# Optimization experiments

Hardware: AMD Instinct MI355X
Metric: run time of the kernel (lower is better)

Reference implementation:

```python
import jax, jax.numpy as jnp
import numpy as np

N_NODES = 100000
N_EDGES = 3200000
N_GRAPHS = 128
F_IN, HID, N_CLS = 3, 64, 6


def setup_inputs() -> dict:
    key = jax.random.key(0)
    ks = jax.random.split(key, 9)
    x = jax.random.normal(ks[0], (N_NODES, F_IN), dtype=jnp.float32)
    edge_index = jax.random.randint(ks[1], (2, N_EDGES), 0, N_NODES, dtype=jnp.int32)
    batch = jnp.sort(jax.random.randint(ks[2], (N_NODES,), 0, N_GRAPHS, dtype=jnp.int32))
    # GCNConv weights (glorot-ish) and biases
    W1 = jax.random.normal(ks[3], (F_IN, HID), dtype=jnp.float32) / np.float32(np.sqrt(F_IN))
    b1 = jnp.zeros((HID,), dtype=jnp.float32)
    W2 = jax.random.normal(ks[4], (HID, HID), dtype=jnp.float32) / np.float32(np.sqrt(HID))
    b2 = jnp.zeros((HID,), dtype=jnp.float32)
    Wl = jax.random.normal(ks[5], (HID, N_CLS), dtype=jnp.float32) / np.float32(np.sqrt(HID))
    bl = jnp.zeros((N_CLS,), dtype=jnp.float32)
    return {"x": x, "edge_index": edge_index, "batch": batch,
            "W1": W1, "b1": b1, "W2": W2, "b2": b2, "Wl": Wl, "bl": bl}


def _gcn_forward(x, edge_index, batch, W1, b1, W2, b2, Wl, bl):
    n = x.shape[0]
    # add self-loops (PyG GCNConv default)
    loop = jnp.arange(n, dtype=edge_index.dtype)
    src = jnp.concatenate([edge_index[0], loop])
    dst = jnp.concatenate([edge_index[1], loop])
    # symmetric normalization D^{-1/2} (A+I) D^{-1/2}
    deg = jax.ops.segment_sum(jnp.ones_like(dst, dtype=x.dtype), dst, num_segments=n)
    dis = jax.lax.rsqrt(jnp.maximum(deg, 1.0))
    norm = dis[src] * dis[dst]  # [E+N]

    def conv(h, W, b):
        h = h @ W                                   # [N, out]
        msg = h[src] * norm[:, None]                # gather + scale
        agg = jax.ops.segment_sum(msg, dst, num_segments=n)  # scatter-add
        return agg + b

    h = jax.nn.relu(conv(x, W1, b1))
    h = jax.nn.relu(conv(h, W2, b2))
    # global mean pool over graphs
    ones = jnp.ones((n,), dtype=h.dtype)
    cnt = jax.ops.segment_sum(ones, batch, num_segments=N_GRAPHS)
    pooled = jax.ops.segment_sum(h, batch, num_segments=N_GRAPHS) / jnp.maximum(cnt, 1.0)[:, None]
    logits = pooled @ Wl + bl
    return jax.nn.log_softmax(logits, axis=1)


def reference(x, edge_index, batch, W1, b1, W2, b2, Wl, bl):
    return _gcn_forward(x, edge_index, batch, W1, b1, W2, b2, Wl, bl)
```

## Files before the change

### kernel.cpp

```cpp
#include <hip/hip_runtime.h>
#include <math.h>

#define NGRAPH 128
#define NPB 128
#define CAPB 6144
#define PSL 8
#define MMN 16
#define TILEA 16384
#define EPTA 16


__device__ inline unsigned char f2fp8(float f) {
    float a = fabsf(f);
    unsigned s = (__float_as_uint(f) >> 31) << 7;
    if (!(a > 0.f)) return (unsigned char)s;
    if (a >= 448.f) return (unsigned char)(s | 0x7e);
    int e = (int)(__float_as_uint(a) >> 23) - 127;
    if (e < -6) e = -6;
    float sc = __uint_as_float((unsigned)(130 - e) << 23);
    int q = (int)rintf(a * sc);
    if (q >= 16) { e += 1; q = 8; }
    if (q <= 0) return (unsigned char)s;
    unsigned expb, man;
    if (q < 8) { expb = 0; man = (unsigned)q; }
    else { expb = (unsigned)(e + 7); man = (unsigned)(q - 8); }
    return (unsigned char)(s | (expb << 3) | man);
}

typedef float v2f __attribute__((ext_vector_type(2)));

__device__ inline void fp8x4_dec(unsigned u, float* o) {
#pragma unroll
    for (int k = 0; k < 4; ++k) {
        unsigned b = (u >> (8 * k)) & 0xffu;
        unsigned bits = ((b & 0x80u) << 24) | ((b & 0x7fu) << 20);
        o[k] = __uint_as_float(bits) * 0x1p+120f;
    }
}

__device__ inline void acc16(uint4 u, float w, v2f* a) {
#if __has_builtin(__builtin_amdgcn_cvt_pk_f32_fp8)
    v2f ws; ws.x = w; ws.y = w;
    a[0] += __builtin_amdgcn_cvt_pk_f32_fp8(u.x, false) * ws;
    a[1] += __builtin_amdgcn_cvt_pk_f32_fp8(u.x, true)  * ws;
    a[2] += __builtin_amdgcn_cvt_pk_f32_fp8(u.y, false) * ws;
    a[3] += __builtin_amdgcn_cvt_pk_f32_fp8(u.y, true)  * ws;
    a[4] += __builtin_amdgcn_cvt_pk_f32_fp8(u.z, false) * ws;
    a[5] += __builtin_amdgcn_cvt_pk_f32_fp8(u.z, true)  * ws;
    a[6] += __builtin_amdgcn_cvt_pk_f32_fp8(u.w, false) * ws;
    a[7] += __builtin_amdgcn_cvt_pk_f32_fp8(u.w, true)  * ws;
#else
    float* af = (float*)a;
    unsigned uu[4] = {u.x, u.y, u.z, u.w};
#pragma unroll
    for (int q = 0; q < 4; ++q) {
        float d[4]; fp8x4_dec(uu[q], d);
#pragma unroll
        for (int k = 0; k < 4; ++k) af[q * 4 + k] += d[k] * w;
    }
#endif
}


__global__ void init_k(int* __restrict__ cursorF, float* __restrict__ pooled, int NBF) {
    int i = blockIdx.x * blockDim.x + threadIdx.x;
    if (i < NBF) cursorF[i] = i * CAPB;
    if (i < NGRAPH * 64) pooled[i] = 0.0f;
}


__global__ __launch_bounds__(1024) void binA_k(const int* __restrict__ src,
        const int* __restrict__ dst, int* cursorF, unsigned* __restrict__ binned,
        int E, int NBF) {
    __shared__ int lh[1024];
    __shared__ int startv[1024];
    __shared__ int gdelta[1024];
    __shared__ unsigned lout[TILEA];
    int tid = threadIdx.x;
    lh[tid] = 0;
    __syncthreads();
    int base = blockIdx.x * TILEA;
    int d[EPTA];
    int s[EPTA];
#pragma unroll
    for (int u = 0; u < EPTA; ++u) {
        int e = base + tid + u * 1024;
        d[u] = (e < E) ? dst[e] : -1;
        s[u] = (e < E) ? src[e] : 0;
    }
#pragma unroll
    for (int u = 0; u < EPTA; ++u)
        if (d[u] >= 0) atomicAdd(&lh[d[u] >> 7], 1);
    __syncthreads();
    if (tid <= NBF) startv[tid] = (tid == 0) ? 0 : lh[tid - 1];
    __syncthreads();
    for (int off = 1; off <= NBF; off <<= 1) {
        int v = 0;
        if (tid <= NBF && tid >= off) v = startv[tid - off];
        __syncthreads();
        if (tid <= NBF && tid >= off) startv[tid] += v;
        __syncthreads();
    }
    if (tid < NBF) {
        int cnt = lh[tid];
        int g = cnt ? atomicAdd(&cursorF[tid], cnt) : 0;
        gdelta[tid] = g - startv[tid];
        lh[tid] = startv[tid];
    }
    __syncthreads();
#pragma unroll
    for (int u = 0; u < EPTA; ++u) {
        if (d[u] >= 0) {
            int p = atomicAdd(&lh[d[u] >> 7], 1);
            lout[p] = (unsigned)s[u] | ((unsigned)(d[u] & (NPB - 1)) << 17);
        }
    }
    __syncthreads();
    int wv = tid >> 6, ln = tid & 63;
    for (int bkt = wv; bkt < NBF; bkt += 16) {
        int ls = startv[bkt], le = lh[bkt];
        int gd = gdelta[bkt];
        for (int i = ls + ln; i < le; i += 64)
            binned[gd + i] = lout[i];
    }
}


__global__ __launch_bounds__(256) void reorder_k(unsigned* __restrict__ binned,
        const int* __restrict__ cursorF, int* __restrict__ nodebeg,
        int* __restrict__ nodeend, float* __restrict__ dis,
        const float* __restrict__ x, float* __restrict__ xs, int n) {
    __shared__ int hist[NPB + 1];
    __shared__ int startv[NPB + 1];
    __shared__ unsigned lout[CAPB];
    int tid = threadIdx.x;
    int b = blockIdx.x;
    int beg = b * CAPB, end = cursorF[b];
    int total = end - beg;
    if (tid <= NPB) hist[tid] = 0;
    __syncthreads();
    for (int i = beg + tid; i < end; i += 256)
        atomicAdd(&hist[binned[i] >> 17], 1);
    __syncthreads();
    if (tid < NPB) startv[tid + 1] = hist[tid];
    if (tid == 0) startv[0] = 0;
    __syncthreads();
    for (int off = 1; off <= NPB; off <<= 1) {
        int v = 0;
        if (tid <= NPB && tid >= off) v = startv[tid - off];
        __syncthreads();
        if (tid <= NPB && tid >= off) startv[tid] += v;
        __syncthreads();
    }
    if (tid < NPB) hist[tid] = startv[tid];
    __syncthreads();
    for (int i = beg + tid; i < end; i += 256) {
        unsigned r = binned[i];
        int p = atomicAdd(&hist[r >> 17], 1);
        lout[p] = r & 0x1FFFFu;
    }
    __syncthreads();
    for (int jj = tid; jj < total; jj += 256)
        binned[beg + jj] = lout[jj];
    int node0 = b * NPB;
    if (tid < NPB) {
        int node = node0 + tid;
        if (node < n) {
            nodebeg[node] = beg + startv[tid];
            nodeend[node] = beg + startv[tid + 1];
            int deg = startv[tid + 1] - startv[tid];
            float d = rsqrtf((float)deg + 1.0f);
            dis[node] = d;
            xs[node * 3]     = x[node * 3] * d;
            xs[node * 3 + 1] = x[node * 3 + 1] * d;
            xs[node * 3 + 2] = x[node * 3 + 2] * d;
        }
    }
}


__global__ __launch_bounds__(256) void mm12_k(const float* __restrict__ xs,
        const int* __restrict__ nodebeg, const int* __restrict__ nodeend,
        const int* __restrict__ csr, const float* __restrict__ dis,
        const float* __restrict__ W1, const float* __restrict__ b1,
        const float* __restrict__ W2, unsigned char* __restrict__ tb, int n) {
    __shared__ __attribute__((aligned(16))) float hrow[4][64];
    __shared__ float4 ytile[MMN];
    int tid = threadIdx.x;
    int j = tid & 63;

    float w1r0 = W1[j], w1r1 = W1[64 + j], w1r2 = W1[128 + j], bbr = b1[j];
    float wreg[64];
#pragma unroll
    for (int k = 0; k < 64; ++k) wreg[k] = W2[k * 64 + j];

    int ns = tid >> 4;
    int el = tid & 15;
    int gnode = blockIdx.x * MMN + ns;
    float a0 = 0.f, a1 = 0.f, a2 = 0.f;
    float dn = 0.f;
    int b = 0, e = 0;
    if (gnode < n) {
        dn = dis[gnode];
        b = nodebeg[gnode];
        e = nodeend[gnode];
    }
    for (int i = b + el; i < e; i += 32) {
        int s0 = csr[i];
        int i1 = i + 16;
        bool v1 = i1 < e;
        int s1 = v1 ? csr[i1] : s0;
        float m1 = v1 ? 1.f : 0.f;
        float p0 = xs[s0 * 3], p1 = xs[s0 * 3 + 1], p2 = xs[s0 * 3 + 2];
        float q0 = xs[s1 * 3], q1 = xs[s1 * 3 + 1], q2 = xs[s1 * 3 + 2];
        a0 += p0 + q0 * m1;
        a1 += p1 + q1 * m1;
        a2 += p2 + q2 * m1;
    }
#pragma unroll
    for (int off = 1; off <= 8; off <<= 1) {
        a0 += __shfl_xor(a0, off);
        a1 += __shfl_xor(a1, off);
        a2 += __shfl_xor(a2, off);
    }
    if (el == 0 && gnode < n) {
        ytile[ns] = make_float4(dn * (a0 + xs[gnode * 3]),
                                dn * (a1 + xs[gnode * 3 + 1]),
                                dn * (a2 + xs[gnode * 3 + 2]), dn);
    }
    __syncthreads();

    int nl = tid >> 6;
    for (int it = 0; it < MMN / 4; ++it) {
        int slot = it * 4 + nl;
        int node = blockIdx.x * MMN + slot;
        float4 yv = ytile[slot];
        float h = fmaxf(yv.x * w1r0 + yv.y * w1r1 + yv.z * w1r2 + bbr, 0.0f);
        hrow[nl][j] = h;
        __builtin_amdgcn_wave_barrier();
        float acc = 0.0f;
#pragma unroll
        for (int k = 0; k < 64; k += 4) {
            float4 h4 = *(const float4*)&hrow[nl][k];
            acc += h4.x * wreg[k + 0];
            acc += h4.y * wreg[k + 1];
            acc += h4.z * wreg[k + 2];
            acc += h4.w * wreg[k + 3];
        }
        if (node < n) tb[node * 64 + j] = f2fp8(acc * yv.w);
        __builtin_amdgcn_wave_barrier();
    }
}


__global__ __launch_bounds__(256) void gather2_k(const unsigned char* __restrict__ tb,
        const float* __restrict__ b2, const int* __restrict__ nodebeg,
        const int* __restrict__ nodeend, const int* __restrict__ csr,
        const float* __restrict__ dis, float* __restrict__ agg, int n) {
    int g = blockIdx.x * blockDim.x + threadIdx.x;
    int node = g >> 5;
    if (node >= n) return;
    int l32 = threadIdx.x & 31;
    int c4 = l32 & 3, esub = l32 >> 2;
    const uint4* t16 = (const uint4*)tb;
    float dn = dis[node];
    int b = nodebeg[node], e = nodeend[node];
    v2f av[8];
#pragma unroll
    for (int k = 0; k < 8; ++k) { av[k].x = 0.f; av[k].y = 0.f; }
    for (int i = b; i < e + 1; i += 64) {
        int i0 = i + esub;
        int s0 = (i0      < e) ? csr[i0]      : node;
        int s1 = (i0 + 8  < e) ? csr[i0 + 8]  : node;
        int s2 = (i0 + 16 < e) ? csr[i0 + 16] : node;
        int s3 = (i0 + 24 < e) ? csr[i0 + 24] : node;
        int s4 = (i0 + 32 < e) ? csr[i0 + 32] : node;
        int s5 = (i0 + 40 < e) ? csr[i0 + 40] : node;
        int s6 = (i0 + 48 < e) ? csr[i0 + 48] : node;
        int s7 = (i0 + 56 < e) ? csr[i0 + 56] : node;
        uint4 u0 = t16[s0 * 4 + c4];
        uint4 u1 = t16[s1 * 4 + c4];
        uint4 u2 = t16[s2 * 4 + c4];
        uint4 u3 = t16[s3 * 4 + c4];
        uint4 u4 = t16[s4 * 4 + c4];
        uint4 u5 = t16[s5 * 4 + c4];
        uint4 u6 = t16[s6 * 4 + c4];
        uint4 u7 = t16[s7 * 4 + c4];
        acc16(u0, (i0      <= e) ? 1.f : 0.f, av);
        acc16(u1, (i0 + 8  <= e) ? 1.f : 0.f, av);
        acc16(u2, (i0 + 16 <= e) ? 1.f : 0.f, av);
        acc16(u3, (i0 + 24 <= e) ? 1.f : 0.f, av);
        acc16(u4, (i0 + 32 <= e) ? 1.f : 0.f, av);
        acc16(u5, (i0 + 40 <= e) ? 1.f : 0.f, av);
        acc16(u6, (i0 + 48 <= e) ? 1.f : 0.f, av);
        acc16(u7, (i0 + 56 <= e) ? 1.f : 0.f, av);
    }
    float* a = (float*)av;
    {
        bool hi = (esub & 1) != 0;
#pragma unroll
        for (int t = 0; t < 8; ++t) {
            float send = hi ? a[t] : a[8 + t];
            float r = __shfl_xor(send, 4);
            a[t] = (hi ? a[8 + t] : a[t]) + r;
        }
    }
    {
        bool hi = (esub & 2) != 0;
#pragma unroll
        for (int t = 0; t < 4; ++t) {
            float send = hi ? a[t] : a[4 + t];
            float r = __shfl_xor(send, 8);
            a[t] = (hi ? a[4 + t] : a[t]) + r;
        }
    }
    {
        bool hi = (esub & 4) != 0;
#pragma unroll
        for (int t = 0; t < 2; ++t) {
            float send = hi ? a[t] : a[2 + t];
            float r = __shfl_xor(send, 16);
            a[t] = (hi ? a[2 + t] : a[t]) + r;
        }
    }
    int cb = ((esub & 1) << 3) | ((esub & 2) << 1) | ((esub & 4) >> 1);
    int ch = c4 * 16 + cb;
    v2f bv = *(const v2f*)&b2[ch];
    v2f outv;
    outv.x = dn * a[0] + bv.x;
    outv.y = dn * a[1] + bv.y;
    *(v2f*)&agg[node * 64 + ch] = outv;
}


__device__ inline int lower_bound_i(const int* a, int n, int key) {
    int lo = 0, hi = n;
    while (lo < hi) {
        int mid = (lo + hi) >> 1;
        if (a[mid] < key) lo = mid + 1; else hi = mid;
    }
    return lo;
}

__global__ void pool_k(const float* __restrict__ agg2, const int* __restrict__ batch,
                       float* __restrict__ pooled, int n) {
    int g = blockIdx.x / PSL, slice = blockIdx.x % PSL;
    int start = lower_bound_i(batch, n, g);
    int end   = lower_bound_i(batch, n, g + 1);
    int len = end - start;
    int cb = start + (int)(((long long)len * slice) / PSL);
    int ce = start + (int)(((long long)len * (slice + 1)) / PSL);
    int wid = threadIdx.x >> 6, lane = threadIdx.x & 63;
    float acc = 0.0f;
    for (int i = cb + wid; i < ce; i += 4)
        acc += fmaxf(agg2[i * 64 + lane], 0.0f);
    __shared__ float red[4][64];
    red[wid][lane] = acc;
    __syncthreads();
    if (threadIdx.x < 64) {
        float s = red[0][lane] + red[1][lane] + red[2][lane] + red[3][lane];
        atomicAdd(&pooled[g * 64 + lane], s);
    }
}

__global__ void head_k(const float* __restrict__ pooled, const int* __restrict__ batch,
                       const float* __restrict__ Wl, const float* __restrict__ bl,
                       float* __restrict__ out, int n) {
    int g = blockIdx.x, t = threadIdx.x;
    __shared__ float p[64];
    __shared__ float logit[8];
    int start = lower_bound_i(batch, n, g);
    int end   = lower_bound_i(batch, n, g + 1);
    float cnt = fmaxf((float)(end - start), 1.0f);
    p[t] = pooled[g * 64 + t] / cnt;
    __syncthreads();
    if (t < 6) {
        float a = bl[t];
        for (int k = 0; k < 64; ++k) a += p[k] * Wl[k * 6 + t];
        logit[t] = a;
    }
    __syncthreads();
    if (t == 0) {
        float m = logit[0];
        for (int j = 1; j < 6; ++j) m = fmaxf(m, logit[j]);
        float s = 0.0f;
        for (int j = 0; j < 6; ++j) s += expf(logit[j] - m);
        float lse = m + logf(s);
        for (int j = 0; j < 6; ++j) out[g * 6 + j] = logit[j] - lse;
    }
}


extern "C" void kernel_launch(void* const* d_in, const int* in_sizes, int n_in,
                              void* d_out, int out_size, void* d_ws, size_t ws_size,
                              hipStream_t stream) {
    const float* x     = (const float*)d_in[0];
    const int*   ei    = (const int*)d_in[1];
    const int*   batch = (const int*)d_in[2];
    const float* W1    = (const float*)d_in[3];
    const float* b1    = (const float*)d_in[4];
    const float* W2    = (const float*)d_in[5];
    const float* b2    = (const float*)d_in[6];
    const float* Wl    = (const float*)d_in[7];
    const float* bl    = (const float*)d_in[8];

    int n = in_sizes[0] / 3;
    int E = in_sizes[1] / 2;
    const int* src = ei;
    const int* dst = ei + E;

    int NBF = (n + NPB - 1) / NPB;
    int GA = (E + TILEA - 1) / TILEA;

    char* ws = (char*)d_ws;
    size_t o = 0;
    auto alloc = [&](size_t bytes) -> void* {
        void* p = ws + o;
        o += (bytes + 255) & ~(size_t)255;
        return p;
    };
    int*      cursorF = (int*)alloc((size_t)NBF * 4);
    float*    dis     = (float*)alloc((size_t)n * 4);
    int*      nodebeg = (int*)alloc((size_t)n * 4);
    int*      nodeend = (int*)alloc((size_t)n * 4);
    float*    xs      = (float*)alloc((size_t)n * 3 * 4);
    float*    pooled  = (float*)alloc((size_t)NGRAPH * 64 * 4);
    unsigned* binned  = (unsigned*)alloc((size_t)NBF * CAPB * 4);
    unsigned char* tb = (unsigned char*)alloc((size_t)n * 64);
    float*    agg     = (float*)alloc((size_t)n * 64 * 4);
    float*    out = (float*)d_out;

    int initN = NGRAPH * 64;
    init_k<<<(initN + 255) / 256, 256, 0, stream>>>(cursorF, pooled, NBF);
    binA_k<<<GA, 1024, 0, stream>>>(src, dst, cursorF, binned, E, NBF);
    reorder_k<<<NBF, 256, 0, stream>>>(binned, cursorF, nodebeg, nodeend, dis, x, xs, n);

    mm12_k<<<(n + MMN - 1) / MMN, 256, 0, stream>>>(xs, nodebeg, nodeend,
            (const int*)binned, dis, W1, b1, W2, tb, n);
    gather2_k<<<(n * 32 + 255) / 256, 256, 0, stream>>>(tb, b2, nodebeg, nodeend,
            (const int*)binned, dis, agg, n);

    pool_k<<<NGRAPH * PSL, 256, 0, stream>>>(agg, batch, pooled, n);
    head_k<<<NGRAPH, 64, 0, stream>>>(pooled, batch, Wl, bl, out, n);
}
```

Measured before the change: 222.1 us.

## Fuse ReLU and mean-pool accumulation into layer-2 gather kernel

The layer-2 gather kernel now applies ReLU and accumulates node outputs into per-graph sums, using shared-memory bins keyed by batch id followed by global atomics. This removes the separate pool kernel and the full N x 64 fp32 aggregate buffer write and read. The layer-1 gather loop is also unrolled from two to four edges per iteration to increase memory-level parallelism. The cost is more atomic traffic and possible contention on pooled, plus a reliance on batch being sorted so the shared bins cover most nodes.

```diff
diff --git a/kernel.cpp b/kernel.cpp
--- a/kernel.cpp
+++ b/kernel.cpp
@@ -4,7 +4,6 @@
 #define NGRAPH 128
 #define NPB 128
 #define CAPB 6144
-#define PSL 8
 #define MMN 16
 #define TILEA 16384
 #define EPTA 16
@@ -205,17 +204,22 @@
         b = nodebeg[gnode];
         e = nodeend[gnode];
     }
-    for (int i = b + el; i < e; i += 32) {
+    for (int i = b + el; i < e; i += 64) {
+        int i1 = i + 16, i2 = i + 32, i3 = i + 48;
         int s0 = csr[i];
-        int i1 = i + 16;
-        bool v1 = i1 < e;
-        int s1 = v1 ? csr[i1] : s0;
-        float m1 = v1 ? 1.f : 0.f;
+        int s1 = (i1 < e) ? csr[i1] : s0;
+        int s2 = (i2 < e) ? csr[i2] : s0;
+        int s3 = (i3 < e) ? csr[i3] : s0;
+        float m1 = (i1 < e) ? 1.f : 0.f;
+        float m2 = (i2 < e) ? 1.f : 0.f;
+        float m3 = (i3 < e) ? 1.f : 0.f;
         float p0 = xs[s0 * 3], p1 = xs[s0 * 3 + 1], p2 = xs[s0 * 3 + 2];
         float q0 = xs[s1 * 3], q1 = xs[s1 * 3 + 1], q2 = xs[s1 * 3 + 2];
-        a0 += p0 + q0 * m1;
-        a1 += p1 + q1 * m1;
-        a2 += p2 + q2 * m1;
+        float r0 = xs[s2 * 3], r1 = xs[s2 * 3 + 1], r2 = xs[s2 * 3 + 2];
+        float t0 = xs[s3 * 3], t1 = xs[s3 * 3 + 1], t2 = xs[s3 * 3 + 2];
+        a0 += p0 + q0 * m1 + r0 * m2 + t0 * m3;
+        a1 += p1 + q1 * m1 + r1 * m2 + t1 * m3;
+        a2 += p2 + q2 * m1 + r2 * m2 + t2 * m3;
     }
 #pragma unroll
     for (int off = 1; off <= 8; off <<= 1) {
@@ -256,80 +260,101 @@
 __global__ __launch_bounds__(256) void gather2_k(const unsigned char* __restrict__ tb,
         const float* __restrict__ b2, const int* __restrict__ nodebeg,
         const int* __restrict__ nodeend, const int* __restrict__ csr,
-        const float* __restrict__ dis, float* __restrict__ agg, int n) {
-    int g = blockIdx.x * blockDim.x + threadIdx.x;
+        const float* __restrict__ dis, const int* __restrict__ batch,
+        float* __restrict__ pooled, int n) {
+    __shared__ float pacc[4][64];
+    __shared__ int gbase;
+    int tid = threadIdx.x;
+    ((float*)pacc)[tid] = 0.f;
+    int node0 = blockIdx.x * 8;
+    if (tid == 0) gbase = batch[node0 < n ? node0 : (n - 1)];
+    __syncthreads();
+
+    int g = blockIdx.x * blockDim.x + tid;
     int node = g >> 5;
-    if (node >= n) return;
-    int l32 = threadIdx.x & 31;
+    int l32 = tid & 31;
     int c4 = l32 & 3, esub = l32 >> 2;
-    const uint4* t16 = (const uint4*)tb;
-    float dn = dis[node];
-    int b = nodebeg[node], e = nodeend[node];
-    v2f av[8];
-#pragma unroll
-    for (int k = 0; k < 8; ++k) { av[k].x = 0.f; av[k].y = 0.f; }
-    for (int i = b; i < e + 1; i += 64) {
-        int i0 = i + esub;
-        int s0 = (i0      < e) ? csr[i0]      : node;
-        int s1 = (i0 + 8  < e) ? csr[i0 + 8]  : node;
-        int s2 = (i0 + 16 < e) ? csr[i0 + 16] : node;
-        int s3 = (i0 + 24 < e) ? csr[i0 + 24] : node;
-        int s4 = (i0 + 32 < e) ? csr[i0 + 32] : node;
-        int s5 = (i0 + 40 < e) ? csr[i0 + 40] : node;
-        int s6 = (i0 + 48 < e) ? csr[i0 + 48] : node;
-        int s7 = (i0 + 56 < e) ? csr[i0 + 56] : node;
-        uint4 u0 = t16[s0 * 4 + c4];
-        uint4 u1 = t16[s1 * 4 + c4];
-        uint4 u2 = t16[s2 * 4 + c4];
-        uint4 u3 = t16[s3 * 4 + c4];
-        uint4 u4 = t16[s4 * 4 + c4];
-        uint4 u5 = t16[s5 * 4 + c4];
-        uint4 u6 = t16[s6 * 4 + c4];
-        uint4 u7 = t16[s7 * 4 + c4];
-        acc16(u0, (i0      <= e) ? 1.f : 0.f, av);
-        acc16(u1, (i0 + 8  <= e) ? 1.f : 0.f, av);
-        acc16(u2, (i0 + 16 <= e) ? 1.f : 0.f, av);
-        acc16(u3, (i0 + 24 <= e) ? 1.f : 0.f, av);
-        acc16(u4, (i0 + 32 <= e) ? 1.f : 0.f, av);
-        acc16(u5, (i0 + 40 <= e) ? 1.f : 0.f, av);
-        acc16(u6, (i0 + 48 <= e) ? 1.f : 0.f, av);
-        acc16(u7, (i0 + 56 <= e) ? 1.f : 0.f, av);
-    }
-    float* a = (float*)av;
-    {
-        bool hi = (esub & 1) != 0;
-#pragma unroll
-        for (int t = 0; t < 8; ++t) {
-            float send = hi ? a[t] : a[8 + t];
-            float r = __shfl_xor(send, 4);
-            a[t] = (hi ? a[8 + t] : a[t]) + r;
-        }
-    }
-    {
-        bool hi = (esub & 2) != 0;
-#pragma unroll
-        for (int t = 0; t < 4; ++t) {
-            float send = hi ? a[t] : a[4 + t];
-            float r = __shfl_xor(send, 8);
-            a[t] = (hi ? a[4 + t] : a[t]) + r;
-        }
-    }
-    {
-        bool hi = (esub & 4) != 0;
-#pragma unroll
-        for (int t = 0; t < 2; ++t) {
-            float send = hi ? a[t] : a[2 + t];
-            float r = __shfl_xor(send, 16);
-            a[t] = (hi ? a[2 + t] : a[t]) + r;
-        }
-    }
-    int cb = ((esub & 1) << 3) | ((esub & 2) << 1) | ((esub & 4) >> 1);
-    int ch = c4 * 16 + cb;
-    v2f bv = *(const v2f*)&b2[ch];
-    v2f outv;
-    outv.x = dn * a[0] + bv.x;
-    outv.y = dn * a[1] + bv.y;
-    *(v2f*)&agg[node * 64 + ch] = outv;
+    if (node < n) {
+        const uint4* t16 = (const uint4*)tb;
+        float dn = dis[node];
+        int b = nodebeg[node], e = nodeend[node];
+        v2f av[8];
+#pragma unroll
+        for (int k = 0; k < 8; ++k) { av[k].x = 0.f; av[k].y = 0.f; }
+        for (int i = b; i < e + 1; i += 64) {
+            int i0 = i + esub;
+            int s0 = (i0      < e) ? csr[i0]      : node;
+            int s1 = (i0 + 8  < e) ? csr[i0 + 8]  : node;
+            int s2 = (i0 + 16 < e) ? csr[i0 + 16] : node;
+            int s3 = (i0 + 24 < e) ? csr[i0 + 24] : node;
+            int s4 = (i0 + 32 < e) ? csr[i0 + 32] : node;
+            int s5 = (i0 + 40 < e) ? csr[i0 + 40] : node;
+            int s6 = (i0 + 48 < e) ? csr[i0 + 48] : node;
+            int s7 = (i0 + 56 < e) ? csr[i0 + 56] : node;
+            uint4 u0 = t16[s0 * 4 + c4];
+            uint4 u1 = t16[s1 * 4 + c4];
+            uint4 u2 = t16[s2 * 4 + c4];
+            uint4 u3 = t16[s3 * 4 + c4];
+            uint4 u4 = t16[s4 * 4 + c4];
+            uint4 u5 = t16[s5 * 4 + c4];
+            uint4 u6 = t16[s6 * 4 + c4];
+            uint4 u7 = t16[s7 * 4 + c4];
+            acc16(u0, (i0      <= e) ? 1.f : 0.f, av);
+            acc16(u1, (i0 + 8  <= e) ? 1.f : 0.f, av);
+            acc16(u2, (i0 + 16 <= e) ? 1.f : 0.f, av);
+            acc16(u3, (i0 + 24 <= e) ? 1.f : 0.f, av);
+            acc16(u4, (i0 + 32 <= e) ? 1.f : 0.f, av);
+            acc16(u5, (i0 + 40 <= e) ? 1.f : 0.f, av);
+            acc16(u6, (i0 + 48 <= e) ? 1.f : 0.f, av);
+            acc16(u7, (i0 + 56 <= e) ? 1.f : 0.f, av);
+        }
+        float* a = (float*)av;
+        {
+            bool hi = (esub & 1) != 0;
+#pragma unroll
+            for (int t = 0; t < 8; ++t) {
+                float send = hi ? a[t] : a[8 + t];
+                float r = __shfl_xor(send, 4);
+                a[t] = (hi ? a[8 + t] : a[t]) + r;
+            }
+        }
+        {
+            bool hi = (esub & 2) != 0;
+#pragma unroll
+            for (int t = 0; t < 4; ++t) {
+                float send = hi ? a[t] : a[4 + t];
+                float r = __shfl_xor(send, 8);
+                a[t] = (hi ? a[4 + t] : a[t]) + r;
+            }
+        }
+        {
+            bool hi = (esub & 4) != 0;
+#pragma unroll
+            for (int t = 0; t < 2; ++t) {
+                float send = hi ? a[t] : a[2 + t];
+                float r = __shfl_xor(send, 16);
+                a[t] = (hi ? a[2 + t] : a[t]) + r;
+            }
+        }
+        int cb = ((esub & 1) << 3) | ((esub & 2) << 1) | ((esub & 4) >> 1);
+        int ch = c4 * 16 + cb;
+        v2f bv = *(const v2f*)&b2[ch];
+        float v0 = fmaxf(dn * a[0] + bv.x, 0.f);
+        float v1 = fmaxf(dn * a[1] + bv.y, 0.f);
+        int gid = batch[node];
+        int bin = gid - gbase;
+        if (bin < 4) {
+            atomicAdd(&pacc[bin][ch], v0);
+            atomicAdd(&pacc[bin][ch + 1], v1);
+        } else {
+            atomicAdd(&pooled[gid * 64 + ch], v0);
+            atomicAdd(&pooled[gid * 64 + ch + 1], v1);
+        }
+    }
+    __syncthreads();
+    int fbin = tid >> 6, fch = tid & 63;
+    float fv = pacc[fbin][fch];
+    if (fv != 0.f) atomicAdd(&pooled[(gbase + fbin) * 64 + fch], fv);
 }
 
 
@@ -340,27 +365,6 @@
         if (a[mid] < key) lo = mid + 1; else hi = mid;
     }
     return lo;
-}
-
-__global__ void pool_k(const float* __restrict__ agg2, const int* __restrict__ batch,
-                       float* __restrict__ pooled, int n) {
-    int g = blockIdx.x / PSL, slice = blockIdx.x % PSL;
-    int start = lower_bound_i(batch, n, g);
-    int end   = lower_bound_i(batch, n, g + 1);
-    int len = end - start;
-    int cb = start + (int)(((long long)len * slice) / PSL);
-    int ce = start + (int)(((long long)len * (slice + 1)) / PSL);
-    int wid = threadIdx.x >> 6, lane = threadIdx.x & 63;
-    float acc = 0.0f;
-    for (int i = cb + wid; i < ce; i += 4)
-        acc += fmaxf(agg2[i * 64 + lane], 0.0f);
-    __shared__ float red[4][64];
-    red[wid][lane] = acc;
-    __syncthreads();
-    if (threadIdx.x < 64) {
-        float s = red[0][lane] + red[1][lane] + red[2][lane] + red[3][lane];
-        atomicAdd(&pooled[g * 64 + lane], s);
-    }
 }
 
 __global__ void head_k(const float* __restrict__ pooled, const int* __restrict__ batch,
@@ -427,7 +431,6 @@
     float*    pooled  = (float*)alloc((size_t)NGRAPH * 64 * 4);
     unsigned* binned  = (unsigned*)alloc((size_t)NBF * CAPB * 4);
     unsigned char* tb = (unsigned char*)alloc((size_t)n * 64);
-    float*    agg     = (float*)alloc((size_t)n * 64 * 4);
     float*    out = (float*)d_out;
 
     int initN = NGRAPH * 64;
@@ -438,8 +441,7 @@
     mm12_k<<<(n + MMN - 1) / MMN, 256, 0, stream>>>(xs, nodebeg, nodeend,
             (const int*)binned, dis, W1, b1, W2, tb, n);
     gather2_k<<<(n * 32 + 255) / 256, 256, 0, stream>>>(tb, b2, nodebeg, nodeend,
-            (const int*)binned, dis, agg, n);
-
-    pool_k<<<NGRAPH * PSL, 256, 0, stream>>>(agg, batch, pooled, n);
+            (const int*)binned, dis, batch, pooled, n);
+
     head_k<<<NGRAPH, 64, 0, stream>>>(pooled, batch, Wl, bl, out, n);
 }
```

New measurement: 219.0 us, median of 2. Within noise of the previous version (-1.4%).
